# Kernel optimization log

Measured on AMD Instinct MI355X. Metric: run time of the kernel, lower is better.

The kernel has to match this reference:

```python
import jax, jax.numpy as jnp
import numpy as np

F0 = 64            # n_filter
NC = 4             # n_calls
NL = 4             # n_layers for image_size=128
CF = 3             # sobel perception factor: [sobel_x, sobel_y, identity]
FIN = F0 * CF      # 192
FH = F0            # 64 hidden
FOUT = 2 * F0      # 128 (gated)
LRELU_SLOPE = 0.2

# constant depthwise kernels (buffers in torch, not trainable)
_gx = np.array([[-1., 0., 1.], [-2., 0., 2.], [-1., 0., 1.]], np.float32) / 8.0
_gy = _gx.T.copy()
_g1 = np.exp(-0.5 * np.array([-1., 0., 1.]) ** 2)
_gk = np.outer(_g1, _g1)
_gk = (_gk / _gk.sum()).astype(np.float32)   # 3x3 gaussian, sigma=1


def _dw3x3(x, k):
    # depthwise 3x3 conv, same kernel per channel, pad=1
    C = x.shape[1]
    kern = jnp.broadcast_to(jnp.asarray(k, x.dtype), (C, 1, 3, 3))
    return jax.lax.conv_general_dilated(
        x, kern, (1, 1), [(1, 1), (1, 1)],
        dimension_numbers=('NCHW', 'OIHW', 'NCHW'), feature_group_count=C)


def _inorm(x, eps=1e-5):
    m = x.mean((2, 3), keepdims=True)
    v = ((x - m) ** 2).mean((2, 3), keepdims=True)
    return (x - m) * jax.lax.rsqrt(v + eps)


def _lrelu(x):
    return jax.nn.leaky_relu(x, LRELU_SLOPE)


def _c11(x, w, b=None):
    # shared 1x1 conv: w [Co,Ci]
    y = jnp.einsum('oi,bihw->bohw', w, x)
    return y if b is None else y + b[None, :, None, None]


def _bc11(x, w, b):
    # per-sample 1x1 conv: w [B,Co,Ci], b [B,Co]
    return jnp.einsum('boi,bihw->bohw', w, x) + b[:, :, None, None]


def _dyna(p, latc, dw, db):
    # hypernetwork: latc [B,512] -> per-sample residual-block 1x1 conv weights
    B = latc.shape[0]
    ks = jnp.einsum('bi,pi->bp', latc, dw) + db
    i0 = FH * FIN; i1 = i0 + FH; i2 = i1 + FOUT * FH
    i3 = i2 + FOUT; i4 = i3 + FOUT * FIN
    w0 = ks[:, :i0].reshape(B, FH, FIN);  b0 = ks[:, i0:i1]
    w1 = ks[:, i1:i2].reshape(B, FOUT, FH); b1 = ks[:, i2:i3]
    ws = ks[:, i3:i4].reshape(B, FOUT, FIN); bs = ks[:, i4:]
    x_s = _bc11(p, ws, bs)
    dx = _bc11(_lrelu(p), w0, b0)
    dx = _bc11(_lrelu(dx), w1, b1)
    return x_s + 0.1 * dx


def _forward(lat, seed, leak_factor, lat_exp_w, lat_exp_b, noise_w,
             dyna_w, dyna_b, conv0_w, conv0_b, conv1_w, conv1_b, convs_w,
             out_w, out_b):
    B = lat.shape[0]
    out = jnp.broadcast_to(seed, (B,) + seed.shape[1:])   # [B,64,16,16]
    lf = jnp.clip(leak_factor, 1e-3, 1e3)
    nkey = jax.random.key(7)
    for c in range(NL * NC):   # 16 structural steps, resolution doubles every NC
        # perception: depthwise sobel + identity -> [B, 3*F0, H, W]
        p = jnp.concatenate([_dw3x3(out, _gx), _dw3x3(out, _gy), out], axis=1)
        p = _inorm(p)
        # shared residual block (1x1 convs)
        xs = _c11(p, convs_w)
        dx = _c11(_lrelu(p), conv0_w, conv0_b)
        dx = _c11(_lrelu(dx), conv1_w, conv1_b)
        f = xs + 0.1 * dx
        # per-step latent expansion (torch Linear: x @ W.T + b)
        latc = jnp.einsum('bi,oi->bo', lat, lat_exp_w[c]) + lat_exp_b[c]
        d = _dyna(p, latc, dyna_w, dyna_b)
        o = f + d                                  # [B, 2*F0, H, W]
        a, g = jnp.split(o, 2, axis=1)
        o = a * jax.nn.sigmoid(g)                  # gated
        # noise injection (stylegan-style, per-channel learned weight)
        noise = jax.random.normal(jax.random.fold_in(nkey, c),
                                  (B, 1) + o.shape[2:], o.dtype)
        o = o + noise_w[c][None, :, None, None] * noise
        out = out + lf * o
        if c < NL * NC - 1 and c % NC == NC - 1:
            Bc, Cc, H, W = out.shape
            out = jax.image.resize(out, (Bc, Cc, 2 * H, 2 * W), method='bilinear')
            out = _dw3x3(out, _gk)                 # gaussian smoothing
    out_raw = _c11(out, out_w, out_b)              # 1x1 out conv -> [B,3,128,128]
    return jnp.clip(out_raw, -1.0, 1.0), out_raw


def setup_inputs() -> dict:
    key = jax.random.key(0)
    ks = jax.random.split(key, 16)
    B, LAT = 8, 512
    P = FH * FIN + FH + FOUT * FH + FOUT + FOUT * FIN + FOUT   # 45376
    r = lambda k, shp, s: jax.random.normal(k, shp, jnp.float32) * s
    return {
        'lat': r(ks[0], (B, LAT), 1.0),
        'seed': r(ks[1], (1, F0, 16, 16), 1.0),
        'leak_factor': jnp.float32(0.1),
        'lat_exp_w': r(ks[2], (NL * NC, LAT, LAT), LAT ** -0.5),
        'lat_exp_b': jnp.zeros((NL * NC, LAT), jnp.float32),
        'noise_w': r(ks[3], (NL * NC, F0), 0.1),
        'dyna_w': r(ks[4], (P, LAT), 2e-3),
        'dyna_b': jnp.zeros((P,), jnp.float32),
        'conv0_w': r(ks[5], (FH, FIN), FIN ** -0.5),
        'conv0_b': jnp.zeros((FH,), jnp.float32),
        'conv1_w': r(ks[6], (FOUT, FH), FH ** -0.5),
        'conv1_b': jnp.zeros((FOUT,), jnp.float32),
        'convs_w': r(ks[7], (FOUT, FIN), FIN ** -0.5),
        'out_w': r(ks[8], (3, F0), F0 ** -0.5),
        'out_b': jnp.zeros((3,), jnp.float32),
    }


def reference(lat, seed, leak_factor, lat_exp_w, lat_exp_b, noise_w,
              dyna_w, dyna_b, conv0_w, conv0_b, conv1_w, conv1_b, convs_w,
              out_w, out_b):
    return _forward(lat, seed, leak_factor, lat_exp_w, lat_exp_b, noise_w,
                    dyna_w, dyna_b, conv0_w, conv0_b, conv1_w, conv1_b,
                    convs_w, out_w, out_b)
```

## Files before the change

kernel.cpp:

```cpp
#include <hip/hip_runtime.h>
#include <cstdint>
#include <cstddef>
#include <cmath>

#define DI __device__ __forceinline__

constexpr int B_ = 8;
constexpr int F0_ = 64;
constexpr int LAT_ = 512;
constexpr int P_ = 45376;
constexpr int NLAY_ = 16;

typedef __attribute__((ext_vector_type(8))) short short8;
typedef __attribute__((ext_vector_type(4))) float f32x4;

constexpr int WPK_STRIDE = 90112;
constexpr int WPK_W1B = 24576;
constexpr int WPK_WS  = 49152;
constexpr int WPK_W2  = 73728;

constexpr size_t OFF_PART   = 0;
constexpr size_t OFF_B3     = 98304;
constexpr size_t OFF_LATCBF = 139264;
constexpr size_t OFF_OUT0   = 172032;
constexpr size_t OFF_OUT1   = 8560640;
constexpr size_t OFF_WPK    = 16949248;

DI uint16_t f2bf(float f) {
  uint32_t u = __float_as_uint(f);
  uint32_t r = (u + 0x7FFFu + ((u >> 16) & 1u)) >> 16;
  return (uint16_t)r;
}
DI uint32_t pk2bf(float a, float b) {
  return (uint32_t)f2bf(a) | ((uint32_t)f2bf(b) << 16);
}

DI void tf_cipher(uint32_t k0, uint32_t k1, uint32_t x0, uint32_t x1,
                  uint32_t& o0, uint32_t& o1) {
  const uint32_t ks2 = k0 ^ k1 ^ 0x1BD11BDAu;
  uint32_t a = x0 + k0, b = x1 + k1;
#define TFR(r) { a += b; b = (b << (r)) | (b >> (32 - (r))); b ^= a; }
  TFR(13) TFR(15) TFR(26) TFR(6)  a += k1;  b += ks2 + 1u;
  TFR(17) TFR(29) TFR(16) TFR(24) a += ks2; b += k0 + 2u;
  TFR(13) TFR(15) TFR(26) TFR(6)  a += k0;  b += k1 + 3u;
  TFR(17) TFR(29) TFR(16) TFR(24) a += k1;  b += ks2 + 4u;
  TFR(13) TFR(15) TFR(26) TFR(6)  a += ks2; b += k0 + 5u;
#undef TFR
  o0 = a; o1 = b;
}

static void host_tf_cipher(uint32_t k0, uint32_t k1, uint32_t x0, uint32_t x1,
                           uint32_t& o0, uint32_t& o1) {
  const uint32_t ks2 = k0 ^ k1 ^ 0x1BD11BDAu;
  uint32_t a = x0 + k0, b = x1 + k1;
#define TFR(r) { a += b; b = (b << (r)) | (b >> (32 - (r))); b ^= a; }
  TFR(13) TFR(15) TFR(26) TFR(6)  a += k1;  b += ks2 + 1u;
  TFR(17) TFR(29) TFR(16) TFR(24) a += ks2; b += k0 + 2u;
  TFR(13) TFR(15) TFR(26) TFR(6)  a += k0;  b += k1 + 3u;
  TFR(17) TFR(29) TFR(16) TFR(24) a += k1;  b += ks2 + 4u;
  TFR(13) TFR(15) TFR(26) TFR(6)  a += ks2; b += k0 + 5u;
#undef TFR
  o0 = a; o1 = b;
}

DI float erfinv_f(float x) {
  float w = -log1pf(-x * x);
  float p;
  if (w < 5.0f) {
    w = w - 2.5f;
    p = 2.81022636e-08f;
    p = fmaf(p, w, 3.43273939e-07f);
    p = fmaf(p, w, -3.5233877e-06f);
    p = fmaf(p, w, -4.39150654e-06f);
    p = fmaf(p, w, 0.00021858087f);
    p = fmaf(p, w, -0.00125372503f);
    p = fmaf(p, w, -0.00417768164f);
    p = fmaf(p, w, 0.246640727f);
    p = fmaf(p, w, 1.50140941f);
  } else {
    w = sqrtf(w) - 3.0f;
    p = -0.000200214257f;
    p = fmaf(p, w, 0.000100950558f);
    p = fmaf(p, w, 0.00134934322f);
    p = fmaf(p, w, -0.00367342844f);
    p = fmaf(p, w, 0.00573950773f);
    p = fmaf(p, w, -0.0076224613f);
    p = fmaf(p, w, 0.00943887047f);
    p = fmaf(p, w, 1.00167406f);
    p = fmaf(p, w, 2.83297682f);
  }
  return p * x;
}

DI float noise_val(uint32_t k0, uint32_t k1, uint32_t idx) {
  uint32_t o0, o1;
  tf_cipher(k0, k1, 0u, idx, o0, o1);
  uint32_t bits = o0 ^ o1;
  float f = __uint_as_float((bits >> 9) | 0x3f800000u) - 1.0f;
  const float lo = -0.99999994f;
  float u = fmaxf(lo, fmaf(f, 2.0f, lo));
  return 1.41421354f * erfinv_f(u);
}

__global__ __launch_bounds__(256) void k_seed(const float* __restrict__ seed,
                                              float* __restrict__ outb) {
  const int idx = blockIdx.x * 256 + threadIdx.x;
  const int px = (idx >> 6) & 255, ch = idx & 63;
  outb[idx] = seed[ch * 256 + px];
}

__global__ __launch_bounds__(256) void k_latc(const float* __restrict__ lat,
                                              const float* __restrict__ wexp,
                                              const float* __restrict__ bexp,
                                              unsigned short* __restrict__ latc_bf) {
  const int c = blockIdx.x;
  const int tid = threadIdx.x;
  __shared__ float latS[B_][LAT_];
  for (int i = tid; i < B_ * LAT_; i += 256) latS[i >> 9][i & 511] = lat[i];
  __syncthreads();
  for (int o = tid; o < LAT_; o += 256) {
    float acc[B_] = {0, 0, 0, 0, 0, 0, 0, 0};
    const float* wr = wexp + ((size_t)c * LAT_ + o) * LAT_;
    for (int k = 0; k < LAT_; k += 4) {
      float4 w4 = *(const float4*)(wr + k);
#pragma unroll
      for (int b = 0; b < B_; ++b) {
        acc[b] = fmaf(w4.x, latS[b][k + 0], acc[b]);
        acc[b] = fmaf(w4.y, latS[b][k + 1], acc[b]);
        acc[b] = fmaf(w4.z, latS[b][k + 2], acc[b]);
        acc[b] = fmaf(w4.w, latS[b][k + 3], acc[b]);
      }
    }
    const float bb = bexp[c * LAT_ + o];
#pragma unroll
    for (int b = 0; b < B_; ++b)
      latc_bf[((size_t)c * B_ + b) * LAT_ + o] = f2bf(acc[b] + bb);
  }
}

__global__ __launch_bounds__(256) void k_wstatic(const float* __restrict__ conv0_w,
                                                 const float* __restrict__ conv1_w,
                                                 unsigned short* __restrict__ wpk) {
  const int cb = blockIdx.x;
  unsigned short* wq = wpk + (size_t)cb * WPK_STRIDE;
  for (int i = threadIdx.x; i < 64 * 192; i += 256) {
    const float v = conv0_w[i];
    wq[i] = f2bf(0.6f * v);
    wq[WPK_W1B + i] = f2bf(0.4f * v);
  }
  for (int i = threadIdx.x; i < 128 * 64; i += 256) {
    int oc = i >> 6, k = i & 63;
    wq[WPK_W2 + oc * 128 + k] = f2bf(0.1f * conv1_w[i]);
  }
}

__global__ __launch_bounds__(256) void k_ks(
    const unsigned short* __restrict__ latc_bf,
    const float* __restrict__ dyna_w,
    const float* __restrict__ dyna_b,
    const float* __restrict__ convs_w,
    unsigned short* __restrict__ wpk,
    float* __restrict__ bias3) {
  const int n0 = blockIdx.x * 64;
  const int tid = threadIdx.x;
  const int wv = tid >> 6, lane = tid & 63, lg = lane >> 4, lr = lane & 15;
  __shared__ __align__(16) unsigned char AsB[128 * 64];
  __shared__ __align__(16) unsigned char BsB[64 * 64];

  f32x4 acc[2][4];
#pragma unroll
  for (int i = 0; i < 2; ++i)
#pragma unroll
    for (int j = 0; j < 4; ++j) acc[i][j] = (f32x4)0.f;

  const int am = tid >> 1, ah = tid & 1;
  const int bn = tid >> 2, bq = tid & 3;

  for (int kc = 0; kc < LAT_; kc += 32) {
    __syncthreads();
    {
      const uint4* src = (const uint4*)(latc_bf + (size_t)am * LAT_ + kc + ah * 16);
      const uint4 u0 = src[0];
      const uint4 u1 = src[1];
      const int swz = (am & 7) << 4;
      *(uint4*)(AsB + ((am * 64 + ah * 32) ^ swz)) = u0;
      *(uint4*)(AsB + ((am * 64 + ah * 32 + 16) ^ swz)) = u1;
    }
    {
      const float* src = dyna_w + (size_t)(n0 + bn) * LAT_ + kc + bq * 8;
      const float4 f0 = *(const float4*)(src);
      const float4 f1 = *(const float4*)(src + 4);
      uint4 u;
      u.x = pk2bf(f0.x, f0.y);
      u.y = pk2bf(f0.z, f0.w);
      u.z = pk2bf(f1.x, f1.y);
      u.w = pk2bf(f1.z, f1.w);
      *(uint4*)(BsB + ((bn * 64 + bq * 16) ^ ((bn & 7) << 4))) = u;
    }
    __syncthreads();
    short8 af[2], bfx[4];
#pragma unroll
    for (int mt = 0; mt < 2; ++mt) {
      const int rm = wv * 32 + mt * 16 + lr;
      af[mt] = *(const short8*)(AsB + ((rm * 64 + lg * 16) ^ ((rm & 7) << 4)));
    }
#pragma unroll
    for (int nt = 0; nt < 4; ++nt) {
      const int rn = nt * 16 + lr;
      bfx[nt] = *(const short8*)(BsB + ((rn * 64 + lg * 16) ^ ((rn & 7) << 4)));
    }
#pragma unroll
    for (int mt = 0; mt < 2; ++mt)
#pragma unroll
      for (int nt = 0; nt < 4; ++nt)
        acc[mt][nt] = __builtin_amdgcn_mfma_f32_16x16x32_bf16(af[mt], bfx[nt], acc[mt][nt], 0, 0, 0);
  }

#pragma unroll
  for (int nt = 0; nt < 4; ++nt) {
    const int n = n0 + nt * 16 + lr;
    int typ, e_off;
    float addv = 0.f;
    if (n < 12288) { int oc = n / 192; int k = n - oc * 192; typ = 0; e_off = (64 + oc) * 192 + k; }
    else if (n < 12352) { typ = 1; e_off = n - 12288; }
    else if (n < 20544) { int m2 = n - 12352; typ = 2; e_off = WPK_W2 + (m2 >> 6) * 128 + 64 + (m2 & 63); }
    else if (n < 20672) { typ = 3; e_off = 64 + (n - 20544); }
    else if (n < 45248) {
      int m3 = n - 20672; int oc = m3 / 192; int k = m3 - oc * 192;
      typ = 4; e_off = WPK_WS + oc * 192 + k; addv = convs_w[oc * 192 + k];
    } else { typ = 5; e_off = 192 + (n - 45248); }
    const float db = dyna_b[n];
#pragma unroll
    for (int mt = 0; mt < 2; ++mt) {
#pragma unroll
      for (int reg = 0; reg < 4; ++reg) {
        const int cb = wv * 32 + mt * 16 + lg * 4 + reg;
        float v = acc[mt][nt][reg] + db;
        if (typ == 4) v += addv;
        if (typ == 2) v *= 0.1f;
        if (typ == 0) {
          wpk[(size_t)cb * WPK_STRIDE + e_off] = f2bf(0.6f * v);
          wpk[(size_t)cb * WPK_STRIDE + WPK_W1B + e_off] = f2bf(0.4f * v);
        } else if (typ == 2 || typ == 4) {
          wpk[(size_t)cb * WPK_STRIDE + e_off] = f2bf(v);
        } else {
          bias3[(size_t)cb * 320 + e_off] = v;
        }
      }
    }
  }
}

__global__ __launch_bounds__(256) void k_stats1(const float* __restrict__ cur,
                                                float* __restrict__ part,
                                                int H, int W, int logW, int HW,
                                                int NS) {
  const int b = blockIdx.y;
  const int strip = blockIdx.x;
  const int tid = threadIdx.x;
  const int chq = tid & 15, pxo = (tid >> 4) & 3, wv = tid >> 6;
  const int pxs = HW / NS;
  const int p0 = strip * pxs;
  const float* __restrict__ ob = cur + (size_t)b * HW * 64 + chq * 4;
  const f32x4 zf = (f32x4)0.f;

  f32x4 s[6];
#pragma unroll
  for (int i = 0; i < 6; ++i) s[i] = zf;

  for (int px = p0 + (wv * 4 + pxo); px < p0 + pxs; px += 16) {
    const int h = px >> logW, w = px & (W - 1);
    const bool vu = h > 0, vd = h < H - 1, vl = w > 0, vr = w < W - 1;
    const float* bp = ob + (size_t)px * 64;
    const int rW = W * 64;
    f32x4 c00 = (vu && vl) ? *(const f32x4*)(bp - rW - 64) : zf;
    f32x4 c01 = vu         ? *(const f32x4*)(bp - rW)      : zf;
    f32x4 c02 = (vu && vr) ? *(const f32x4*)(bp - rW + 64) : zf;
    f32x4 c10 = vl         ? *(const f32x4*)(bp - 64)      : zf;
    f32x4 c11 =              *(const f32x4*)(bp);
    f32x4 c12 = vr         ? *(const f32x4*)(bp + 64)      : zf;
    f32x4 c20 = (vd && vl) ? *(const f32x4*)(bp + rW - 64) : zf;
    f32x4 c21 = vd         ? *(const f32x4*)(bp + rW)      : zf;
    f32x4 c22 = (vd && vr) ? *(const f32x4*)(bp + rW + 64) : zf;
    const f32x4 t0 = c22 - c00, t1 = c02 - c20;
    const f32x4 vx = (t0 + t1 + 2.f * (c12 - c10)) * 0.125f;
    const f32x4 vy = (t0 - t1 + 2.f * (c21 - c01)) * 0.125f;
    s[0] += vx; s[1] += vx * vx;
    s[2] += vy; s[3] += vy * vy;
    s[4] += c11; s[5] += c11 * c11;
  }
#pragma unroll
  for (int i = 0; i < 6; ++i)
#pragma unroll
    for (int c = 0; c < 4; ++c) {
      s[i][c] += __shfl_xor(s[i][c], 16, 64);
      s[i][c] += __shfl_xor(s[i][c], 32, 64);
    }
  __shared__ f32x4 redS[64][6];
  if ((tid & 63) < 16) {
#pragma unroll
    for (int i = 0; i < 6; ++i) redS[wv * 16 + chq][i] = s[i];
  }
  __syncthreads();
  if (tid < 16) {
    f32x4 a[6];
#pragma unroll
    for (int i = 0; i < 6; ++i)
      a[i] = redS[tid][i] + redS[16 + tid][i] + redS[32 + tid][i] + redS[48 + tid][i];
    float* pp = part + (size_t)(b * NS + strip) * 384;
#pragma unroll
    for (int i = 0; i < 6; ++i) {
      const int sec = i >> 1, wbit = i & 1;
#pragma unroll
      for (int c = 0; c < 4; ++c)
        pp[sec * 128 + wbit * 64 + tid * 4 + c] = a[i][c];
    }
  }
}

__global__ __launch_bounds__(256, 4) void k_main(
    const float* __restrict__ cur, float* __restrict__ nxt,
    const float* __restrict__ part,
    const unsigned short* __restrict__ wpk_layer,
    const float* __restrict__ bias3_layer,
    const float* __restrict__ conv0_b,
    const float* __restrict__ conv1_b,
    const float* __restrict__ noise_w_c,
    const float* __restrict__ leak_ptr,
    int HW, int W, int lwpr, int NS, unsigned key0, unsigned key1) {
  const int b = blockIdx.y;
  const int bx = blockIdx.x;
  const int tr = bx >> lwpr, tc = bx & ((1 << lwpr) - 1);
  const int r0 = tr * 4, c0 = tc * 16;
  const int logW = lwpr + 4;
  const int H = HW >> logW;

  const int tid = threadIdx.x;
  const int wv = tid >> 6, lane = tid & 63;
  const int lg = lane >> 4, lr = lane & 15;

  __shared__ __align__(16) unsigned char PrawB[24576];
  __shared__ float mrS[384];
  __shared__ float noiseS[64];
  unsigned short* Hs = (unsigned short*)PrawB;

  const unsigned short* wq = wpk_layer + (size_t)b * WPK_STRIDE;
  const unsigned short* W1A = wq;
  const unsigned short* W1B = wq + WPK_W1B;
  const unsigned short* WS  = wq + WPK_WS;
  const unsigned short* W2  = wq + WPK_W2;
  const float* b3 = bias3_layer + (size_t)b * 320;

  if (tid < 192) {
    const int sec = tid >> 6, ch = tid & 63;
    const float* pb = part + (size_t)b * NS * 384;
    float s1 = 0.f, s2 = 0.f;
    for (int st = 0; st < NS; ++st) {
      s1 += pb[st * 384 + sec * 128 + ch];
      s2 += pb[st * 384 + sec * 128 + 64 + ch];
    }
    const float inv = 1.0f / (float)HW;
    const float m = s1 * inv;
    mrS[sec * 64 + ch] = m;
    mrS[192 + sec * 64 + ch] = rsqrtf(fmaxf(s2 * inv - m * m, 0.f) + 1e-5f);
  }
  if (tid < 64)
    noiseS[tid] = noise_val(key0, key1,
        (unsigned)(b * HW + (r0 + (tid >> 4)) * W + c0 + (tid & 15)));
  __syncthreads();

  {
    const int pxi = lane >> 4;
    const int chq = lane & 15;
    const int ch = chq * 4;
    const int gr = r0 + wv;
    const bool vu = gr > 0, vd = gr < H - 1;
    const int rW = W * 64;
    const f32x4 zf = (f32x4)0.f;
    const f32x4 mx = *(const f32x4*)&mrS[ch];
    const f32x4 rx = *(const f32x4*)&mrS[192 + ch];
    const f32x4 my = *(const f32x4*)&mrS[64 + ch];
    const f32x4 ry = *(const f32x4*)&mrS[192 + 64 + ch];
    const f32x4 mi = *(const f32x4*)&mrS[128 + ch];
    const f32x4 ri = *(const f32x4*)&mrS[192 + 128 + ch];
#pragma unroll
    for (int it = 0; it < 4; ++it) {
      const int cl = it * 4 + pxi;
      const int gc = c0 + cl;
      const bool vl = gc > 0, vr = gc < W - 1;
      const float* bq = cur + ((size_t)b * HW + (size_t)gr * W + gc) * 64 + ch;
      f32x4 c00 = (vu && vl) ? *(const f32x4*)(bq - rW - 64) : zf;
      f32x4 c01 = vu         ? *(const f32x4*)(bq - rW)      : zf;
      f32x4 c02 = (vu && vr) ? *(const f32x4*)(bq - rW + 64) : zf;
      f32x4 c10 = vl         ? *(const f32x4*)(bq - 64)      : zf;
      f32x4 c11 =              *(const f32x4*)(bq);
      f32x4 c12 = vr         ? *(const f32x4*)(bq + 64)      : zf;
      f32x4 c20 = (vd && vl) ? *(const f32x4*)(bq + rW - 64) : zf;
      f32x4 c21 = vd         ? *(const f32x4*)(bq + rW)      : zf;
      f32x4 c22 = (vd && vr) ? *(const f32x4*)(bq + rW + 64) : zf;
      const f32x4 t0 = c22 - c00, t1 = c02 - c20;
      const f32x4 vx = (t0 + t1 + 2.f * (c12 - c10)) * 0.125f;
      const f32x4 vy = (t0 - t1 + 2.f * (c21 - c01)) * 0.125f;
      const f32x4 nx = (vx - mx) * rx;
      const f32x4 ny = (vy - my) * ry;
      const f32x4 ni = (c11 - mi) * ri;
      const int pxl = wv * 16 + cl;
      const int swz = (pxl & 7) << 4;
      const int bb = pxl * 384 + ch * 2;
      uint2 u;
      u.x = pk2bf(nx[0], nx[1]); u.y = pk2bf(nx[2], nx[3]);
      *(uint2*)(PrawB + ((bb) ^ swz)) = u;
      u.x = pk2bf(ny[0], ny[1]); u.y = pk2bf(ny[2], ny[3]);
      *(uint2*)(PrawB + ((bb + 128) ^ swz)) = u;
      u.x = pk2bf(ni[0], ni[1]); u.y = pk2bf(ni[2], ni[3]);
      *(uint2*)(PrawB + ((bb + 256) ^ swz)) = u;
    }
  }
  __syncthreads();

  const int oc0 = 16 * wv;
  const int oc1 = 64 + 16 * wv;
  f32x4 accH[2][4], accO[2][4];
#pragma unroll
  for (int t = 0; t < 2; ++t)
#pragma unroll
    for (int p = 0; p < 4; ++p) { accH[t][p] = (f32x4)0.f; accO[t][p] = (f32x4)0.f; }

#pragma unroll
  for (int kc = 0; kc < 6; ++kc) {
    const int ko = kc * 32 + lg * 8;
    const short8 a1a0 = *(const short8*)(W1A + (size_t)(oc0 + lr) * 192 + ko);
    const short8 a1a1 = *(const short8*)(W1A + (size_t)(oc1 + lr) * 192 + ko);
    const short8 a1b0 = *(const short8*)(W1B + (size_t)(oc0 + lr) * 192 + ko);
    const short8 a1b1 = *(const short8*)(W1B + (size_t)(oc1 + lr) * 192 + ko);
    const short8 as0  = *(const short8*)(WS + (size_t)(oc0 + lr) * 192 + ko);
    const short8 as1  = *(const short8*)(WS + (size_t)(oc1 + lr) * 192 + ko);
#pragma unroll
    for (int pxt = 0; pxt < 4; ++pxt) {
      const int px = pxt * 16 + lr;
      const int byt = (px * 384 + ko * 2) ^ ((px & 7) << 4);
      const short8 br = *(const short8*)(PrawB + byt);
      const short8 babs = br & (short)0x7FFF;
      accO[0][pxt] = __builtin_amdgcn_mfma_f32_16x16x32_bf16(as0, br, accO[0][pxt], 0, 0, 0);
      accO[1][pxt] = __builtin_amdgcn_mfma_f32_16x16x32_bf16(as1, br, accO[1][pxt], 0, 0, 0);
      accH[0][pxt] = __builtin_amdgcn_mfma_f32_16x16x32_bf16(a1a0, br, accH[0][pxt], 0, 0, 0);
      accH[1][pxt] = __builtin_amdgcn_mfma_f32_16x16x32_bf16(a1a1, br, accH[1][pxt], 0, 0, 0);
      accH[0][pxt] = __builtin_amdgcn_mfma_f32_16x16x32_bf16(a1b0, babs, accH[0][pxt], 0, 0, 0);
      accH[1][pxt] = __builtin_amdgcn_mfma_f32_16x16x32_bf16(a1b1, babs, accH[1][pxt], 0, 0, 0);
    }
  }
  __syncthreads();

#pragma unroll
  for (int ti = 0; ti < 2; ++ti) {
    const int ocb = ti ? oc1 : oc0;
    float bh[4];
#pragma unroll
    for (int r = 0; r < 4; ++r) {
      const int oc = ocb + lg * 4 + r;
      bh[r] = (oc < 64) ? conv0_b[oc] : b3[oc - 64];
    }
#pragma unroll
    for (int pxt = 0; pxt < 4; ++pxt) {
      const int px = pxt * 16 + lr;
#pragma unroll
      for (int rp = 0; rp < 2; ++rp) {
        float h0 = accH[ti][pxt][rp * 2 + 0] + bh[rp * 2 + 0];
        float h1 = accH[ti][pxt][rp * 2 + 1] + bh[rp * 2 + 1];
        h0 = fmaxf(h0, 0.2f * h0);
        h1 = fmaxf(h1, 0.2f * h1);
        *(uint32_t*)(&Hs[(size_t)px * 136 + ocb + lg * 4 + rp * 2]) = pk2bf(h0, h1);
      }
    }
  }
  __syncthreads();

#pragma unroll
  for (int kc = 0; kc < 4; ++kc) {
    const int ko = kc * 32 + lg * 8;
    const short8 a20 = *(const short8*)(W2 + (size_t)(oc0 + lr) * 128 + ko);
    const short8 a21 = *(const short8*)(W2 + (size_t)(oc1 + lr) * 128 + ko);
#pragma unroll
    for (int pxt = 0; pxt < 4; ++pxt) {
      const short8 hb = *(const short8*)(&Hs[(size_t)(pxt * 16 + lr) * 136 + ko]);
      accO[0][pxt] = __builtin_amdgcn_mfma_f32_16x16x32_bf16(a20, hb, accO[0][pxt], 0, 0, 0);
      accO[1][pxt] = __builtin_amdgcn_mfma_f32_16x16x32_bf16(a21, hb, accO[1][pxt], 0, 0, 0);
    }
  }

  const float lfv = fminf(fmaxf(leak_ptr[0], 0.001f), 1000.0f);
  float boA[4], boG[4], nw[4];
#pragma unroll
  for (int r = 0; r < 4; ++r) {
    const int oca = oc0 + lg * 4 + r;
    const int ocg = oc1 + lg * 4 + r;
    boA[r] = b3[192 + oca] + 0.1f * (conv1_b[oca] + b3[64 + oca]);
    boG[r] = b3[192 + ocg] + 0.1f * (conv1_b[ocg] + b3[64 + ocg]);
    nw[r] = noise_w_c[oca];
  }
#pragma unroll
  for (int pxt = 0; pxt < 4; ++pxt) {
    const float nz = noiseS[pxt * 16 + lr];
    const size_t adr = ((size_t)b * HW + (size_t)(r0 + pxt) * W + c0 + lr) * 64 + oc0 + lg * 4;
    const f32x4 cv = *(const f32x4*)(cur + adr);
    f32x4 ov;
#pragma unroll
    for (int r = 0; r < 4; ++r) {
      const float a = accO[0][pxt][r] + boA[r];
      const float g = accO[1][pxt][r] + boG[r];
      const float og = a * (1.0f / (1.0f + expf(-g)));
      ov[r] = cv[r] + lfv * (og + nw[r] * nz);
    }
    *(f32x4*)(nxt + adr) = ov;
  }
}

__global__ __launch_bounds__(256) void k_upgauss(const float* __restrict__ src,
                                                 float* __restrict__ dst,
                                                 int H, int W, int loOW, int loOHW,
                                                 float ge, float gm) {
  const int idx = blockIdx.x * 256 + threadIdx.x;
  const int OHW = 1 << loOHW;
  if (idx >= B_ * OHW * 16) return;
  const int chq = idx & 15;
  const int opx = (idx >> 4) & (OHW - 1);
  const int b = idx >> (4 + loOHW);
  const int oh = opx >> loOW, ow = opx & ((1 << loOW) - 1);
  const float g[3] = {ge, gm, ge};

  float wy[3] = {0.f, 0.f, 0.f}, wx[3] = {0.f, 0.f, 0.f};
  const int myi = oh >> 1, mxi = ow >> 1;
#pragma unroll
  for (int d = -1; d <= 1; ++d) {
    {
      const int oo = oh + d;
      if (oo >= 0 && oo < 2 * H) {
        const int i0 = (oo - 1) >> 1;
        const float f = ((oo - 1) & 1) ? 0.75f : 0.25f;
        const int i0c = max(i0, 0), i1c = min(i0 + 1, H - 1);
        wy[i0c - (myi - 1)] += g[d + 1] * (1.f - f);
        wy[i1c - (myi - 1)] += g[d + 1] * f;
      }
    }
    {
      const int oo = ow + d;
      if (oo >= 0 && oo < 2 * W) {
        const int i0 = (oo - 1) >> 1;
        const float f = ((oo - 1) & 1) ? 0.75f : 0.25f;
        const int i0c = max(i0, 0), i1c = min(i0 + 1, W - 1);
        wx[i0c - (mxi - 1)] += g[d + 1] * (1.f - f);
        wx[i1c - (mxi - 1)] += g[d + 1] * f;
      }
    }
  }
  const float* pl = src + ((size_t)b * H * W) * 64 + chq * 4;
  f32x4 acc = (f32x4)0.f;
#pragma unroll
  for (int i = 0; i < 3; ++i) {
    const int ry = min(max(myi - 1 + i, 0), H - 1);
    f32x4 rowv = (f32x4)0.f;
#pragma unroll
    for (int j = 0; j < 3; ++j) {
      const int rx = min(max(mxi - 1 + j, 0), W - 1);
      rowv += wx[j] * *(const f32x4*)(pl + (size_t)(ry * W + rx) * 64);
    }
    acc += wy[i] * rowv;
  }
  *(f32x4*)(dst + ((size_t)b * OHW + opx) * 64 + chq * 4) = acc;
}

__global__ __launch_bounds__(256) void k_final(const float* __restrict__ outbuf,
                                               const float* __restrict__ out_w,
                                               const float* __restrict__ out_b,
                                               float* __restrict__ dout) {
  const int idx = blockIdx.x * 256 + threadIdx.x;
  const int b = idx >> 14, px = idx & 16383;
  const float* src = outbuf + ((size_t)b * 16384 + px) * 64;
  float a0 = out_b[0], a1 = out_b[1], a2 = out_b[2];
  for (int i = 0; i < 64; i += 4) {
    const f32x4 v = *(const f32x4*)(src + i);
    const f32x4 w0 = *(const f32x4*)(out_w + i);
    const f32x4 w1 = *(const f32x4*)(out_w + 64 + i);
    const f32x4 w2 = *(const f32x4*)(out_w + 128 + i);
#pragma unroll
    for (int e = 0; e < 4; ++e) {
      a0 = fmaf(w0[e], v[e], a0);
      a1 = fmaf(w1[e], v[e], a1);
      a2 = fmaf(w2[e], v[e], a2);
    }
  }
  const size_t base = (size_t)b * 49152 + px;
  dout[base] = fminf(fmaxf(a0, -1.f), 1.f);
  dout[base + 16384] = fminf(fmaxf(a1, -1.f), 1.f);
  dout[base + 32768] = fminf(fmaxf(a2, -1.f), 1.f);
  dout[393216 + base] = a0;
  dout[393216 + base + 16384] = a1;
  dout[393216 + base + 32768] = a2;
}

extern "C" void kernel_launch(void* const* d_in, const int* in_sizes, int n_in,
                              void* d_out, int out_size, void* d_ws, size_t ws_size,
                              hipStream_t stream) {
  const float* lat       = (const float*)d_in[0];
  const float* seed      = (const float*)d_in[1];
  const float* leak      = (const float*)d_in[2];
  const float* lat_exp_w = (const float*)d_in[3];
  const float* lat_exp_b = (const float*)d_in[4];
  const float* noise_w   = (const float*)d_in[5];
  const float* dyna_w    = (const float*)d_in[6];
  const float* dyna_b    = (const float*)d_in[7];
  const float* conv0_w   = (const float*)d_in[8];
  const float* conv0_b   = (const float*)d_in[9];
  const float* conv1_w   = (const float*)d_in[10];
  const float* conv1_b   = (const float*)d_in[11];
  const float* convs_w   = (const float*)d_in[12];
  const float* out_w     = (const float*)d_in[13];
  const float* out_b     = (const float*)d_in[14];

  float* wsf = (float*)d_ws;
  float* part = wsf + OFF_PART;
  float* b3   = wsf + OFF_B3;
  unsigned short* latc_bf = (unsigned short*)(wsf + OFF_LATCBF);
  float* out0 = wsf + OFF_OUT0;
  float* out1 = wsf + OFF_OUT1;
  unsigned short* wpk = (unsigned short*)(wsf + OFF_WPK);

  uint32_t lk0[NLAY_], lk1[NLAY_];
  for (int c = 0; c < NLAY_; ++c)
    host_tf_cipher(0u, 7u, 0u, (uint32_t)c, lk0[c], lk1[c]);

  const double ga = exp(-0.5);
  const float ge = (float)(ga / (1.0 + 2.0 * ga));
  const float gm = (float)(1.0 / (1.0 + 2.0 * ga));

  k_seed<<<(B_ * 256 * 64) / 256, 256, 0, stream>>>(seed, out0);
  k_latc<<<NLAY_, 256, 0, stream>>>(lat, lat_exp_w, lat_exp_b, latc_bf);
  k_wstatic<<<NLAY_ * B_, 256, 0, stream>>>(conv0_w, conv1_w, wpk);
  k_ks<<<P_ / 64, 256, 0, stream>>>(latc_bf, dyna_w, dyna_b, convs_w, wpk, b3);

  float* cur = out0;
  float* nxt = out1;
  int H = 16, W = 16, logW = 4;
  for (int c = 0; c < NLAY_; ++c) {
    const int HW = H * W;
    const int NS = (HW >= 16384) ? 32 : ((HW >= 4096) ? 8 : ((HW >= 1024) ? 4 : 1));
    k_stats1<<<dim3(NS, B_), 256, 0, stream>>>(cur, part, H, W, logW, HW, NS);
    k_main<<<dim3(HW / 64, B_), 256, 0, stream>>>(
        cur, nxt, part,
        wpk + (size_t)c * B_ * WPK_STRIDE, b3 + (size_t)c * B_ * 320,
        conv0_b, conv1_b, noise_w + c * F0_, leak,
        HW, W, logW - 4, NS, lk0[c], lk1[c]);
    { float* t = cur; cur = nxt; nxt = t; }
    if ((c & 3) == 3 && c < NLAY_ - 1) {
      const int n1 = B_ * 4 * HW * 16;
      const int loOW = logW + 1, loOHW = 2 * logW + 2;
      k_upgauss<<<(n1 + 255) / 256, 256, 0, stream>>>(cur, nxt, H, W, loOW, loOHW, ge, gm);
      { float* t = cur; cur = nxt; nxt = t; }
      H *= 2; W *= 2; logW += 1;
    }
  }
  k_final<<<(B_ * 16384) / 256, 256, 0, stream>>>(cur, out_w, out_b, (float*)d_out);
  (void)in_sizes; (void)n_in; (void)out_size; (void)ws_size;
}
```

Before: 967.5 us.

## Give each wave its own 16-pixel row and build MFMA operands in registers

The main kernel is restructured so each wave owns one row of 16 pixels and computes all 128 output channels. The normalized Sobel/identity perception is built directly into MFMA B-operand registers instead of being staged through a shared swizzled buffer. The hidden activations go through a small per-wave shared buffer, which removes most block-wide barriers and the large shared staging array. In exchange every wave now loads all weight rows (8 groups) itself, which raises register pressure and weight traffic, and the stats kernel now uses more strips on smaller images.

New measurement: 1.810 ms. +87.1%, slower.

```diff
diff --git a/kernel.cpp b/kernel.cpp
--- a/kernel.cpp
+++ b/kernel.cpp
@@ -251,6 +251,8 @@
   }
 }
 
+DI f32x4 ldc(const float* p, bool c) { return c ? *(const f32x4*)p : (f32x4)0.f; }
+
 __global__ __launch_bounds__(256) void k_stats1(const float* __restrict__ cur,
                                                 float* __restrict__ part,
                                                 int H, int W, int logW, int HW,
@@ -262,29 +264,23 @@
   const int pxs = HW / NS;
   const int p0 = strip * pxs;
   const float* __restrict__ ob = cur + (size_t)b * HW * 64 + chq * 4;
-  const f32x4 zf = (f32x4)0.f;
 
   f32x4 s[6];
 #pragma unroll
-  for (int i = 0; i < 6; ++i) s[i] = zf;
+  for (int i = 0; i < 6; ++i) s[i] = (f32x4)0.f;
 
   for (int px = p0 + (wv * 4 + pxo); px < p0 + pxs; px += 16) {
     const int h = px >> logW, w = px & (W - 1);
     const bool vu = h > 0, vd = h < H - 1, vl = w > 0, vr = w < W - 1;
     const float* bp = ob + (size_t)px * 64;
     const int rW = W * 64;
-    f32x4 c00 = (vu && vl) ? *(const f32x4*)(bp - rW - 64) : zf;
-    f32x4 c01 = vu         ? *(const f32x4*)(bp - rW)      : zf;
-    f32x4 c02 = (vu && vr) ? *(const f32x4*)(bp - rW + 64) : zf;
-    f32x4 c10 = vl         ? *(const f32x4*)(bp - 64)      : zf;
-    f32x4 c11 =              *(const f32x4*)(bp);
-    f32x4 c12 = vr         ? *(const f32x4*)(bp + 64)      : zf;
-    f32x4 c20 = (vd && vl) ? *(const f32x4*)(bp + rW - 64) : zf;
-    f32x4 c21 = vd         ? *(const f32x4*)(bp + rW)      : zf;
-    f32x4 c22 = (vd && vr) ? *(const f32x4*)(bp + rW + 64) : zf;
-    const f32x4 t0 = c22 - c00, t1 = c02 - c20;
-    const f32x4 vx = (t0 + t1 + 2.f * (c12 - c10)) * 0.125f;
-    const f32x4 vy = (t0 - t1 + 2.f * (c21 - c01)) * 0.125f;
+    const f32x4 c11 = *(const f32x4*)(bp);
+    f32x4 vx = ldc(bp - rW + 64, vu && vr) - ldc(bp - rW - 64, vu && vl)
+             + 2.f * (ldc(bp + 64, vr) - ldc(bp - 64, vl))
+             + ldc(bp + rW + 64, vd && vr) - ldc(bp + rW - 64, vd && vl);
+    f32x4 vy = ldc(bp + rW - 64, vd && vl) + 2.f * ldc(bp + rW, vd) + ldc(bp + rW + 64, vd && vr)
+             - ldc(bp - rW - 64, vu && vl) - 2.f * ldc(bp - rW, vu) - ldc(bp - rW + 64, vu && vr);
+    vx *= 0.125f; vy *= 0.125f;
     s[0] += vx; s[1] += vx * vx;
     s[2] += vy; s[3] += vy * vy;
     s[4] += c11; s[5] += c11 * c11;
@@ -339,10 +335,8 @@
   const int wv = tid >> 6, lane = tid & 63;
   const int lg = lane >> 4, lr = lane & 15;
 
-  __shared__ __align__(16) unsigned char PrawB[24576];
   __shared__ float mrS[384];
-  __shared__ float noiseS[64];
-  unsigned short* Hs = (unsigned short*)PrawB;
+  __shared__ __align__(16) unsigned short HsAll[4][16 * 138];
 
   const unsigned short* wq = wpk_layer + (size_t)b * WPK_STRIDE;
   const unsigned short* W1A = wq;
@@ -364,152 +358,109 @@
     mrS[sec * 64 + ch] = m;
     mrS[192 + sec * 64 + ch] = rsqrtf(fmaxf(s2 * inv - m * m, 0.f) + 1e-5f);
   }
-  if (tid < 64)
-    noiseS[tid] = noise_val(key0, key1,
-        (unsigned)(b * HW + (r0 + (tid >> 4)) * W + c0 + (tid & 15)));
   __syncthreads();
 
-  {
-    const int pxi = lane >> 4;
-    const int chq = lane & 15;
-    const int ch = chq * 4;
-    const int gr = r0 + wv;
-    const bool vu = gr > 0, vd = gr < H - 1;
-    const int rW = W * 64;
-    const f32x4 zf = (f32x4)0.f;
-    const f32x4 mx = *(const f32x4*)&mrS[ch];
-    const f32x4 rx = *(const f32x4*)&mrS[192 + ch];
-    const f32x4 my = *(const f32x4*)&mrS[64 + ch];
-    const f32x4 ry = *(const f32x4*)&mrS[192 + 64 + ch];
-    const f32x4 mi = *(const f32x4*)&mrS[128 + ch];
-    const f32x4 ri = *(const f32x4*)&mrS[192 + 128 + ch];
-#pragma unroll
-    for (int it = 0; it < 4; ++it) {
-      const int cl = it * 4 + pxi;
-      const int gc = c0 + cl;
-      const bool vl = gc > 0, vr = gc < W - 1;
-      const float* bq = cur + ((size_t)b * HW + (size_t)gr * W + gc) * 64 + ch;
-      f32x4 c00 = (vu && vl) ? *(const f32x4*)(bq - rW - 64) : zf;
-      f32x4 c01 = vu         ? *(const f32x4*)(bq - rW)      : zf;
-      f32x4 c02 = (vu && vr) ? *(const f32x4*)(bq - rW + 64) : zf;
-      f32x4 c10 = vl         ? *(const f32x4*)(bq - 64)      : zf;
-      f32x4 c11 =              *(const f32x4*)(bq);
-      f32x4 c12 = vr         ? *(const f32x4*)(bq + 64)      : zf;
-      f32x4 c20 = (vd && vl) ? *(const f32x4*)(bq + rW - 64) : zf;
-      f32x4 c21 = vd         ? *(const f32x4*)(bq + rW)      : zf;
-      f32x4 c22 = (vd && vr) ? *(const f32x4*)(bq + rW + 64) : zf;
-      const f32x4 t0 = c22 - c00, t1 = c02 - c20;
-      const f32x4 vx = (t0 + t1 + 2.f * (c12 - c10)) * 0.125f;
-      const f32x4 vy = (t0 - t1 + 2.f * (c21 - c01)) * 0.125f;
-      const f32x4 nx = (vx - mx) * rx;
-      const f32x4 ny = (vy - my) * ry;
-      const f32x4 ni = (c11 - mi) * ri;
-      const int pxl = wv * 16 + cl;
-      const int swz = (pxl & 7) << 4;
-      const int bb = pxl * 384 + ch * 2;
-      uint2 u;
-      u.x = pk2bf(nx[0], nx[1]); u.y = pk2bf(nx[2], nx[3]);
-      *(uint2*)(PrawB + ((bb) ^ swz)) = u;
-      u.x = pk2bf(ny[0], ny[1]); u.y = pk2bf(ny[2], ny[3]);
-      *(uint2*)(PrawB + ((bb + 128) ^ swz)) = u;
-      u.x = pk2bf(ni[0], ni[1]); u.y = pk2bf(ni[2], ni[3]);
-      *(uint2*)(PrawB + ((bb + 256) ^ swz)) = u;
-    }
-  }
-  __syncthreads();
-
-  const int oc0 = 16 * wv;
-  const int oc1 = 64 + 16 * wv;
-  f32x4 accH[2][4], accO[2][4];
-#pragma unroll
-  for (int t = 0; t < 2; ++t)
-#pragma unroll
-    for (int p = 0; p < 4; ++p) { accH[t][p] = (f32x4)0.f; accO[t][p] = (f32x4)0.f; }
+  const int gr = r0 + wv;
+  const int gc = c0 + lr;
+  const bool vu = gr > 0, vd = gr < H - 1, vl = gc > 0, vr = gc < W - 1;
+  const float* rowb = cur + ((size_t)b * HW + (size_t)gr * W + gc) * 64;
+  const int rW = W * 64;
+  const float nzv = noise_val(key0, key1, (unsigned)(b * HW + gr * W + gc));
+
+  f32x4 accH[8], accO[8];
+#pragma unroll
+  for (int g = 0; g < 8; ++g) { accH[g] = (f32x4)0.f; accO[g] = (f32x4)0.f; }
 
 #pragma unroll
   for (int kc = 0; kc < 6; ++kc) {
-    const int ko = kc * 32 + lg * 8;
-    const short8 a1a0 = *(const short8*)(W1A + (size_t)(oc0 + lr) * 192 + ko);
-    const short8 a1a1 = *(const short8*)(W1A + (size_t)(oc1 + lr) * 192 + ko);
-    const short8 a1b0 = *(const short8*)(W1B + (size_t)(oc0 + lr) * 192 + ko);
-    const short8 a1b1 = *(const short8*)(W1B + (size_t)(oc1 + lr) * 192 + ko);
-    const short8 as0  = *(const short8*)(WS + (size_t)(oc0 + lr) * 192 + ko);
-    const short8 as1  = *(const short8*)(WS + (size_t)(oc1 + lr) * 192 + ko);
-#pragma unroll
-    for (int pxt = 0; pxt < 4; ++pxt) {
-      const int px = pxt * 16 + lr;
-      const int byt = (px * 384 + ko * 2) ^ ((px & 7) << 4);
-      const short8 br = *(const short8*)(PrawB + byt);
-      const short8 babs = br & (short)0x7FFF;
-      accO[0][pxt] = __builtin_amdgcn_mfma_f32_16x16x32_bf16(as0, br, accO[0][pxt], 0, 0, 0);
-      accO[1][pxt] = __builtin_amdgcn_mfma_f32_16x16x32_bf16(as1, br, accO[1][pxt], 0, 0, 0);
-      accH[0][pxt] = __builtin_amdgcn_mfma_f32_16x16x32_bf16(a1a0, br, accH[0][pxt], 0, 0, 0);
-      accH[1][pxt] = __builtin_amdgcn_mfma_f32_16x16x32_bf16(a1a1, br, accH[1][pxt], 0, 0, 0);
-      accH[0][pxt] = __builtin_amdgcn_mfma_f32_16x16x32_bf16(a1b0, babs, accH[0][pxt], 0, 0, 0);
-      accH[1][pxt] = __builtin_amdgcn_mfma_f32_16x16x32_bf16(a1b1, babs, accH[1][pxt], 0, 0, 0);
-    }
-  }
-  __syncthreads();
-
-#pragma unroll
-  for (int ti = 0; ti < 2; ++ti) {
-    const int ocb = ti ? oc1 : oc0;
-    float bh[4];
-#pragma unroll
-    for (int r = 0; r < 4; ++r) {
-      const int oc = ocb + lg * 4 + r;
-      bh[r] = (oc < 64) ? conv0_b[oc] : b3[oc - 64];
-    }
-#pragma unroll
-    for (int pxt = 0; pxt < 4; ++pxt) {
-      const int px = pxt * 16 + lr;
-#pragma unroll
-      for (int rp = 0; rp < 2; ++rp) {
-        float h0 = accH[ti][pxt][rp * 2 + 0] + bh[rp * 2 + 0];
-        float h1 = accH[ti][pxt][rp * 2 + 1] + bh[rp * 2 + 1];
-        h0 = fmaxf(h0, 0.2f * h0);
-        h1 = fmaxf(h1, 0.2f * h1);
-        *(uint32_t*)(&Hs[(size_t)px * 136 + ocb + lg * 4 + rp * 2]) = pk2bf(h0, h1);
-      }
-    }
-  }
-  __syncthreads();
+    const int ch0 = kc * 32 + lg * 8;
+    const int t = ch0 >> 6;
+    const int oc8 = ch0 & 63;
+    const float* bq = rowb + oc8;
+    f32x4 n0, n1;
+    if (t == 2) {
+      n0 = *(const f32x4*)(bq);
+      n1 = *(const f32x4*)(bq + 4);
+    } else if (t == 0) {
+      n0 = ldc(bq - rW + 64, vu && vr) - ldc(bq - rW - 64, vu && vl)
+         + 2.f * (ldc(bq + 64, vr) - ldc(bq - 64, vl))
+         + ldc(bq + rW + 64, vd && vr) - ldc(bq + rW - 64, vd && vl);
+      n1 = ldc(bq - rW + 68, vu && vr) - ldc(bq - rW - 60, vu && vl)
+         + 2.f * (ldc(bq + 68, vr) - ldc(bq - 60, vl))
+         + ldc(bq + rW + 68, vd && vr) - ldc(bq + rW - 60, vd && vl);
+      n0 *= 0.125f; n1 *= 0.125f;
+    } else {
+      n0 = ldc(bq + rW - 64, vd && vl) + 2.f * ldc(bq + rW, vd) + ldc(bq + rW + 64, vd && vr)
+         - ldc(bq - rW - 64, vu && vl) - 2.f * ldc(bq - rW, vu) - ldc(bq - rW + 64, vu && vr);
+      n1 = ldc(bq + rW - 60, vd && vl) + 2.f * ldc(bq + rW + 4, vd) + ldc(bq + rW + 68, vd && vr)
+         - ldc(bq - rW - 60, vu && vl) - 2.f * ldc(bq - rW + 4, vu) - ldc(bq - rW + 68, vu && vr);
+      n0 *= 0.125f; n1 *= 0.125f;
+    }
+    n0 = (n0 - *(const f32x4*)&mrS[t * 64 + oc8]) * *(const f32x4*)&mrS[192 + t * 64 + oc8];
+    n1 = (n1 - *(const f32x4*)&mrS[t * 64 + oc8 + 4]) * *(const f32x4*)&mrS[192 + t * 64 + oc8 + 4];
+    union { uint32_t u[4]; short8 v; } pc;
+    pc.u[0] = pk2bf(n0[0], n0[1]);
+    pc.u[1] = pk2bf(n0[2], n0[3]);
+    pc.u[2] = pk2bf(n1[0], n1[1]);
+    pc.u[3] = pk2bf(n1[2], n1[3]);
+    const short8 br = pc.v;
+    const short8 babs = br & (short)0x7FFF;
+#pragma unroll
+    for (int g = 0; g < 8; ++g) {
+      const size_t wrow = (size_t)(g * 16 + lr) * 192 + ch0;
+      const short8 a1a = *(const short8*)(W1A + wrow);
+      const short8 a1b = *(const short8*)(W1B + wrow);
+      const short8 asw = *(const short8*)(WS + wrow);
+      accH[g] = __builtin_amdgcn_mfma_f32_16x16x32_bf16(a1a, br, accH[g], 0, 0, 0);
+      accH[g] = __builtin_amdgcn_mfma_f32_16x16x32_bf16(a1b, babs, accH[g], 0, 0, 0);
+      accO[g] = __builtin_amdgcn_mfma_f32_16x16x32_bf16(asw, br, accO[g], 0, 0, 0);
+    }
+  }
+
+  unsigned short* Hs = &HsAll[wv][0];
+#pragma unroll
+  for (int g = 0; g < 8; ++g) {
+    const int ocb = g * 16 + lg * 4;
+    float bh0 = (ocb + 0 < 64) ? conv0_b[ocb + 0] : b3[ocb + 0 - 64];
+    float bh1 = (ocb + 1 < 64) ? conv0_b[ocb + 1] : b3[ocb + 1 - 64];
+    float bh2 = (ocb + 2 < 64) ? conv0_b[ocb + 2] : b3[ocb + 2 - 64];
+    float bh3 = (ocb + 3 < 64) ? conv0_b[ocb + 3] : b3[ocb + 3 - 64];
+    float h0 = accH[g][0] + bh0, h1 = accH[g][1] + bh1;
+    float h2 = accH[g][2] + bh2, h3 = accH[g][3] + bh3;
+    h0 = fmaxf(h0, 0.2f * h0); h1 = fmaxf(h1, 0.2f * h1);
+    h2 = fmaxf(h2, 0.2f * h2); h3 = fmaxf(h3, 0.2f * h3);
+    *(uint32_t*)(&Hs[lr * 138 + ocb])     = pk2bf(h0, h1);
+    *(uint32_t*)(&Hs[lr * 138 + ocb + 2]) = pk2bf(h2, h3);
+  }
 
 #pragma unroll
   for (int kc = 0; kc < 4; ++kc) {
     const int ko = kc * 32 + lg * 8;
-    const short8 a20 = *(const short8*)(W2 + (size_t)(oc0 + lr) * 128 + ko);
-    const short8 a21 = *(const short8*)(W2 + (size_t)(oc1 + lr) * 128 + ko);
-#pragma unroll
-    for (int pxt = 0; pxt < 4; ++pxt) {
-      const short8 hb = *(const short8*)(&Hs[(size_t)(pxt * 16 + lr) * 136 + ko]);
-      accO[0][pxt] = __builtin_amdgcn_mfma_f32_16x16x32_bf16(a20, hb, accO[0][pxt], 0, 0, 0);
-      accO[1][pxt] = __builtin_amdgcn_mfma_f32_16x16x32_bf16(a21, hb, accO[1][pxt], 0, 0, 0);
+    const short8 hb = *(const short8*)(&Hs[lr * 138 + ko]);
+#pragma unroll
+    for (int g = 0; g < 8; ++g) {
+      const short8 a2 = *(const short8*)(W2 + (size_t)(g * 16 + lr) * 128 + ko);
+      accO[g] = __builtin_amdgcn_mfma_f32_16x16x32_bf16(a2, hb, accO[g], 0, 0, 0);
     }
   }
 
   const float lfv = fminf(fmaxf(leak_ptr[0], 0.001f), 1000.0f);
-  float boA[4], boG[4], nw[4];
-#pragma unroll
-  for (int r = 0; r < 4; ++r) {
-    const int oca = oc0 + lg * 4 + r;
-    const int ocg = oc1 + lg * 4 + r;
-    boA[r] = b3[192 + oca] + 0.1f * (conv1_b[oca] + b3[64 + oca]);
-    boG[r] = b3[192 + ocg] + 0.1f * (conv1_b[ocg] + b3[64 + ocg]);
-    nw[r] = noise_w_c[oca];
-  }
-#pragma unroll
-  for (int pxt = 0; pxt < 4; ++pxt) {
-    const float nz = noiseS[pxt * 16 + lr];
-    const size_t adr = ((size_t)b * HW + (size_t)(r0 + pxt) * W + c0 + lr) * 64 + oc0 + lg * 4;
+#pragma unroll
+  for (int g = 0; g < 4; ++g) {
+    const int ocb = g * 16 + lg * 4;
+    const size_t adr = ((size_t)b * HW + (size_t)gr * W + gc) * 64 + ocb;
     const f32x4 cv = *(const f32x4*)(cur + adr);
     f32x4 ov;
 #pragma unroll
     for (int r = 0; r < 4; ++r) {
-      const float a = accO[0][pxt][r] + boA[r];
-      const float g = accO[1][pxt][r] + boG[r];
-      const float og = a * (1.0f / (1.0f + expf(-g)));
-      ov[r] = cv[r] + lfv * (og + nw[r] * nz);
+      const int oca = ocb + r;
+      const int ocg = oca + 64;
+      const float boA = b3[192 + oca] + 0.1f * (conv1_b[oca] + b3[64 + oca]);
+      const float boG = b3[192 + ocg] + 0.1f * (conv1_b[ocg] + b3[64 + ocg]);
+      const float a = accO[g][r] + boA;
+      const float gg = accO[g + 4][r] + boG;
+      const float og = a * (1.0f / (1.0f + expf(-gg)));
+      ov[r] = cv[r] + lfv * (og + noise_w_c[oca] * nzv);
     }
     *(f32x4*)(nxt + adr) = ov;
   }
@@ -643,7 +594,7 @@
   int H = 16, W = 16, logW = 4;
   for (int c = 0; c < NLAY_; ++c) {
     const int HW = H * W;
-    const int NS = (HW >= 16384) ? 32 : ((HW >= 4096) ? 8 : ((HW >= 1024) ? 4 : 1));
+    const int NS = (HW >= 16384) ? 32 : ((HW >= 4096) ? 16 : ((HW >= 1024) ? 8 : 4));
     k_stats1<<<dim3(NS, B_), 256, 0, stream>>>(cur, part, H, W, logW, HW, NS);
     k_main<<<dim3(HW / 64, B_), 256, 0, stream>>>(
         cur, nxt, part,
```
